# Optimization experiments

Hardware: AMD Instinct MI355X
Metric: run time of the kernel (lower is better)

The kernel has to match this reference:

```python
import jax, jax.numpy as jnp
import numpy as np

# ---- static config (matches init_kwargs) ----
IMG = 56        # num_patches = image_size // patch_size = 112 // 2
WIN = 7         # window_size
SHIFT = 3       # shift_size
C = 256         # projection_dim
H = 8           # num_heads
DH = C // H     # head dim = 32
S = WIN * WIN   # tokens per window = 49
NY = IMG // WIN # windows per side = 8
NW = NY * NY    # windows per image = 64
NMLP = 1024
EPS = 1e-5
SCALE = DH ** (-0.5)


def _relative_position_index():
    ch, cw = np.meshgrid(np.arange(WIN), np.arange(WIN), indexing='ij')
    coords = np.stack([ch, cw]).reshape(2, -1)                 # [2, S]
    rel = coords[:, :, None] - coords[:, None, :]              # [2, S, S]
    rel = rel.transpose(1, 2, 0) + (WIN - 1)                   # [S, S, 2]
    idx = rel[:, :, 0] * (2 * WIN - 1) + rel[:, :, 1]          # [S, S]
    return idx.reshape(-1)                                     # [S*S]

REL_IDX = jnp.asarray(_relative_position_index(), dtype=jnp.int32)


def _attn_mask():
    # Faithful replication of the module's mask construction (incl. the empty
    h_slices = (slice(0, -WIN), slice(-WIN, -SHIFT), slice(-SHIFT, None))
    w_slices = (slice(0, -WIN), slice(-WIN, -WIN), slice(-SHIFT, None))
    m = np.zeros((IMG, IMG), dtype=np.float32)
    count = 0
    for hs in h_slices:
        for ws in w_slices:
            m[hs, ws] = count
            count += 1
    mw = m.reshape(NY, WIN, NY, WIN).transpose(0, 2, 1, 3).reshape(NW, S)
    diff = mw[:, None, :] - mw[:, :, None]
    return np.where(diff != 0, -100.0, 0.0).astype(np.float32)  # [NW, S, S]

ATTN_MASK = jnp.asarray(_attn_mask())


def _layernorm(x, gamma, beta):
    mu = jnp.mean(x, axis=-1, keepdims=True)
    var = jnp.mean(jnp.square(x - mu), axis=-1, keepdims=True)
    return (x - mu) * jax.lax.rsqrt(var + EPS) * gamma + beta


def setup_inputs() -> dict:
    key = jax.random.key(0)
    ks = jax.random.split(key, 12)
    B = 32
    s = lambda fan: 1.0 / np.sqrt(fan)
    return {
        'x': jax.random.normal(ks[0], (B, IMG * IMG, C), dtype=jnp.float32),
        'norm_gamma': jnp.ones((C,), jnp.float32),
        'norm_beta': jnp.zeros((C,), jnp.float32),
        'qkv_w': jax.random.normal(ks[1], (C, 3 * C), jnp.float32) * s(C),
        'qkv_b': jnp.zeros((3 * C,), jnp.float32),
        'proj_w': jax.random.normal(ks[2], (C, C), jnp.float32) * s(C),
        'proj_b': jnp.zeros((C,), jnp.float32),
        'rel_bias_table': jax.random.truncated_normal(ks[3], -2.0, 2.0, ((2 * WIN - 1) ** 2, H), jnp.float32) * 0.02,
        'mlp_w1': jax.random.normal(ks[4], (C, NMLP), jnp.float32) * s(C),
        'mlp_b1': jnp.zeros((NMLP,), jnp.float32),
        'mlp_w2': jax.random.normal(ks[5], (NMLP, C), jnp.float32) * s(NMLP),
        'mlp_b2': jnp.zeros((C,), jnp.float32),
    }


def reference(x, norm_gamma, norm_beta, qkv_w, qkv_b, proj_w, proj_b,
              rel_bias_table, mlp_w1, mlp_b1, mlp_w2, mlp_b2):
    B = x.shape[0]
    # ---- shifted-window attention block ----
    shortcut = x
    xn = _layernorm(x, norm_gamma, norm_beta).reshape(B, IMG, IMG, C)
    shifted = jnp.roll(xn, shift=(-SHIFT, -SHIFT), axis=(1, 2))
    # window partition -> [B*NW, S, C]
    xw = shifted.reshape(B, NY, WIN, NY, WIN, C).transpose(0, 1, 3, 2, 4, 5)
    xw = xw.reshape(B * NW, S, C)
    qkv = xw @ qkv_w + qkv_b                                    # [BnW, S, 3C]
    qkv = qkv.reshape(B * NW, S, 3, H, DH).transpose(2, 0, 3, 1, 4)
    q, k, v = qkv[0] * SCALE, qkv[1], qkv[2]                    # [BnW, H, S, DH]
    attn = jnp.einsum('whsd,whtd->whst', q, k)                  # [BnW, H, S, S]
    bias = rel_bias_table[REL_IDX].reshape(S, S, H).transpose(2, 0, 1)
    attn = attn + bias[None]
    attn = attn.reshape(B, NW, H, S, S) + ATTN_MASK[None, :, None]
    attn = jax.nn.softmax(attn.reshape(B * NW, H, S, S), axis=-1)
    out = jnp.einsum('whst,whtd->wshd', attn, v).reshape(B * NW, S, C)
    out = out @ proj_w + proj_b
    # window reverse + unshift
    out = out.reshape(B, NY, NY, WIN, WIN, C).transpose(0, 1, 3, 2, 4, 5)
    out = out.reshape(B, IMG, IMG, C)
    out = jnp.roll(out, shift=(SHIFT, SHIFT), axis=(1, 2)).reshape(B, IMG * IMG, C)
    x = shortcut + out
    # ---- MLP block (same LayerNorm weights reused, as in original) ----
    shortcut2 = x
    xn2 = _layernorm(x, norm_gamma, norm_beta)
    h = jax.nn.gelu(xn2 @ mlp_w1 + mlp_b1, approximate=False)
    h = h @ mlp_w2 + mlp_b2
    return shortcut2 + h
```

## Files before the change

### kernel.cpp

```cpp
#include <hip/hip_runtime.h>
#include <math.h>

#define IMG   56
#define WINSZ 7
#define SHIFTSZ 3
#define CDIM  256
#define NH    8
#define DH    32
#define SEQ   49
#define NYW   8
#define NWIN  64
#define NMLP  1024
#define BATCH 32
#define NTOK  (BATCH*IMG*IMG)
#define BNW   (BATCH*NWIN)
#define SZT   ((size_t)NTOK*CDIM)
#define QSCALE 0.17677669529663687f
#define EPSLN 1e-5f

typedef __attribute__((ext_vector_type(8))) short short8;
typedef __attribute__((ext_vector_type(4))) float f32x4;

__device__ __forceinline__ float bf2f(unsigned short u) {
    union { unsigned i; float f; } c; c.i = ((unsigned)u) << 16; return c.f;
}
__device__ __forceinline__ unsigned short f2bf(float f) {
    union { float f; unsigned i; } c; c.f = f;
    unsigned r = c.i + 0x7fffu + ((c.i >> 16) & 1u);
    return (unsigned short)(r >> 16);
}

__device__ __forceinline__ float gelu_f(float v) {
    float u = v * 0.70710678118654752f;
    float x = fabsf(u);
    float t = __builtin_amdgcn_rcpf(fmaf(0.3275911f, x, 1.0f));
    float e = __expf(-u * u);
    float p = fmaf(1.061405429f, t, -1.453152027f);
    p = fmaf(p, t, 1.421413741f);
    p = fmaf(p, t, -0.284496736f);
    p = fmaf(p, t, 0.254829592f);
    float er = 1.0f - p * t * e;
    er = copysignf(er, u);
    return 0.5f * v * (1.0f + er);
}

#define GLL16(gp, lp) __builtin_amdgcn_global_load_lds( \
    (__attribute__((address_space(1))) void*)(gp),      \
    (__attribute__((address_space(3))) void*)(lp), 16, 0, 0)

__global__ __launch_bounds__(256) void wtrans(const float* __restrict__ in,
                                              unsigned short* __restrict__ out,
                                              int K, int N) {
    int idx = blockIdx.x * 256 + threadIdx.x;
    if (idx >= K * N) return;
    int n = idx / K, k = idx - n * K;
    out[idx] = f2bf(in[(size_t)k * N + n]);
}

template<int WINDOWED>
__global__ __launch_bounds__(256) void ln_kernel(const float* __restrict__ x,
                                                 const float* __restrict__ gamma,
                                                 const float* __restrict__ beta,
                                                 unsigned short* __restrict__ out) {
    int wave = threadIdx.x >> 6;
    int lane = threadIdx.x & 63;
    int tok  = blockIdx.x * 4 + wave;
    int src  = tok;
    if (WINDOWED) {
        int b  = tok / (NWIN * SEQ);
        int r  = tok - b * (NWIN * SEQ);
        int wl = r / SEQ, s = r - wl * SEQ;
        int wy = wl >> 3, wx = wl & 7;
        int i  = s / WINSZ, j = s - i * WINSZ;
        int hp = wy * WINSZ + i + SHIFTSZ; if (hp >= IMG) hp -= IMG;
        int wp = wx * WINSZ + j + SHIFTSZ; if (wp >= IMG) wp -= IMG;
        src = b * (IMG * IMG) + hp * IMG + wp;
    }
    float4 v = *(const float4*)(x + (size_t)src * CDIM + lane * 4);
    float sum = v.x + v.y + v.z + v.w;
    float ss  = v.x*v.x + v.y*v.y + v.z*v.z + v.w*v.w;
#pragma unroll
    for (int off = 32; off; off >>= 1) {
        sum += __shfl_xor(sum, off);
        ss  += __shfl_xor(ss,  off);
    }
    float mu   = sum * (1.0f / CDIM);
    float var  = ss * (1.0f / CDIM) - mu * mu;
    float rstd = rsqrtf(var + EPSLN);
    float4 g  = *(const float4*)(gamma + lane * 4);
    float4 be = *(const float4*)(beta  + lane * 4);
    ushort4 o;
    o.x = f2bf((v.x - mu) * rstd * g.x + be.x);
    o.y = f2bf((v.y - mu) * rstd * g.y + be.y);
    o.z = f2bf((v.z - mu) * rstd * g.z + be.z);
    o.w = f2bf((v.w - mu) * rstd * g.w + be.w);
    *(ushort4*)(out + (size_t)tok * CDIM + lane * 4) = o;
}

#define EPI_QKV  0
#define EPI_PROJ 1
#define EPI_MLP1 2
#define EPI_MLP2 3

template<int EPI>
__global__ __launch_bounds__(256)
void gemm_bt(const unsigned short* __restrict__ A,
             const unsigned short* __restrict__ Bt,
             int K,
             const float* __restrict__ bias,
             const float* __restrict__ resin,
             float* __restrict__ outF,
             unsigned short* __restrict__ outH) {
    __shared__ __align__(16) unsigned short As[128 * 32];
    __shared__ __align__(16) unsigned short Bs[128 * 32];
    int tid  = threadIdx.x;
    int lane = tid & 63, wave = tid >> 6;
    int q4   = lane >> 4, l16 = lane & 15;
    int wm   = wave >> 1, wn = wave & 1;
    int rowBase = blockIdx.y * 128;
    int colBase = blockIdx.x * 128;

    f32x4 acc[4][4];
#pragma unroll
    for (int i = 0; i < 4; i++)
#pragma unroll
        for (int j = 0; j < 4; j++) acc[i][j] = (f32x4){0.f, 0.f, 0.f, 0.f};

    const unsigned short* Ab = A  + (size_t)rowBase * K;
    const unsigned short* Bb = Bt + (size_t)colBase * K;

    int r0 = wave * 32;
    int ra = r0 + (lane >> 2);
    int rb = ra + 16;
    int ca = (lane & 3) ^ ((ra >> 1) & 3);
    int cb = (lane & 3) ^ ((rb >> 1) & 3);
    const size_t off1 = (size_t)ra * K + ca * 8;
    const size_t off2 = (size_t)rb * K + cb * 8;
    unsigned short* ldsA1 = &As[r0 * 32];
    unsigned short* ldsA2 = &As[(r0 + 16) * 32];
    unsigned short* ldsB1 = &Bs[r0 * 32];
    unsigned short* ldsB2 = &Bs[(r0 + 16) * 32];

    for (int k0 = 0; k0 < K; k0 += 32) {
        __syncthreads();
        GLL16(Ab + off1 + k0, ldsA1);
        GLL16(Ab + off2 + k0, ldsA2);
        GLL16(Bb + off1 + k0, ldsB1);
        GLL16(Bb + off2 + k0, ldsB2);
        __syncthreads();
        short8 af[4], bf[4];
#pragma unroll
        for (int mi = 0; mi < 4; mi++) {
            int r = wm * 64 + mi * 16 + l16;
            af[mi] = *(const short8*)&As[r * 32 + ((q4 ^ ((r >> 1) & 3)) * 8)];
        }
#pragma unroll
        for (int ni = 0; ni < 4; ni++) {
            int r = wn * 64 + ni * 16 + l16;
            bf[ni] = *(const short8*)&Bs[r * 32 + ((q4 ^ ((r >> 1) & 3)) * 8)];
        }
#pragma unroll
        for (int mi = 0; mi < 4; mi++)
#pragma unroll
            for (int ni = 0; ni < 4; ni++)
                acc[mi][ni] = __builtin_amdgcn_mfma_f32_16x16x32_bf16(
                    bf[ni], af[mi], acc[mi][ni], 0, 0, 0);
    }

    int mb = rowBase + wm * 64;
    int nb = colBase + wn * 64;
    float4 bias4[4];
#pragma unroll
    for (int ni = 0; ni < 4; ni++)
        bias4[ni] = *(const float4*)(bias + nb + ni * 16 + q4 * 4);

    if (EPI == EPI_QKV) {
        int three = colBase >> 8;
#pragma unroll
        for (int mi = 0; mi < 4; mi++) {
            int m = mb + mi * 16 + l16;
            int w = m / SEQ, s = m - w * SEQ;
#pragma unroll
            for (int ni = 0; ni < 4; ni++) {
                int n0 = nb + ni * 16 + q4 * 4;
                int hh = (n0 >> 5) & 7, dd0 = n0 & 31;
                const float* bp = (const float*)&bias4[ni];
                if (three == 2) {
#pragma unroll
                    for (int r = 0; r < 4; r++)
                        outH[2 * SZT + (((size_t)(w * NH + hh)) * DH + dd0 + r) * 64 + s] =
                            f2bf(acc[mi][ni][r] + bp[r]);
                } else {
                    float sc = (three == 0) ? QSCALE : 1.0f;
                    ushort4 o;
                    o.x = f2bf((acc[mi][ni][0] + bp[0]) * sc);
                    o.y = f2bf((acc[mi][ni][1] + bp[1]) * sc);
                    o.z = f2bf((acc[mi][ni][2] + bp[2]) * sc);
                    o.w = f2bf((acc[mi][ni][3] + bp[3]) * sc);
                    *(ushort4*)(outH + (size_t)three * SZT +
                                (((size_t)(w * NH + hh)) * SEQ + s) * DH + dd0) = o;
                }
            }
        }
    } else if (EPI == EPI_PROJ) {
#pragma unroll
        for (int mi = 0; mi < 4; mi++) {
            int m = mb + mi * 16 + l16;
            int w = m / SEQ, s = m - w * SEQ;
            int b = w >> 6, wl = w & 63;
            int wy = wl >> 3, wx = wl & 7;
            int ii = s / WINSZ, jj = s - ii * WINSZ;
            int hp = wy * WINSZ + ii + SHIFTSZ; if (hp >= IMG) hp -= IMG;
            int wp = wx * WINSZ + jj + SHIFTSZ; if (wp >= IMG) wp -= IMG;
            size_t tok = (size_t)b * (IMG * IMG) + hp * IMG + wp;
#pragma unroll
            for (int ni = 0; ni < 4; ni++) {
                int n0 = nb + ni * 16 + q4 * 4;
                float4 res = *(const float4*)(resin + tok * CDIM + n0);
                float4 o;
                o.x = acc[mi][ni][0] + bias4[ni].x + res.x;
                o.y = acc[mi][ni][1] + bias4[ni].y + res.y;
                o.z = acc[mi][ni][2] + bias4[ni].z + res.z;
                o.w = acc[mi][ni][3] + bias4[ni].w + res.w;
                *(float4*)(outF + tok * CDIM + n0) = o;
            }
        }
    } else if (EPI == EPI_MLP1) {
#pragma unroll
        for (int mi = 0; mi < 4; mi++) {
            int m = mb + mi * 16 + l16;
#pragma unroll
            for (int ni = 0; ni < 4; ni++) {
                int n0 = nb + ni * 16 + q4 * 4;
                ushort4 o;
                o.x = f2bf(gelu_f(acc[mi][ni][0] + bias4[ni].x));
                o.y = f2bf(gelu_f(acc[mi][ni][1] + bias4[ni].y));
                o.z = f2bf(gelu_f(acc[mi][ni][2] + bias4[ni].z));
                o.w = f2bf(gelu_f(acc[mi][ni][3] + bias4[ni].w));
                *(ushort4*)(outH + (size_t)m * NMLP + n0) = o;
            }
        }
    } else {
#pragma unroll
        for (int mi = 0; mi < 4; mi++) {
            int m = mb + mi * 16 + l16;
#pragma unroll
            for (int ni = 0; ni < 4; ni++) {
                int n0 = nb + ni * 16 + q4 * 4;
                float4 res = *(const float4*)(resin + (size_t)m * CDIM + n0);
                float4 o;
                o.x = acc[mi][ni][0] + bias4[ni].x + res.x;
                o.y = acc[mi][ni][1] + bias4[ni].y + res.y;
                o.z = acc[mi][ni][2] + bias4[ni].z + res.z;
                o.w = acc[mi][ni][3] + bias4[ni].w + res.w;
                *(float4*)(outF + (size_t)m * CDIM + n0) = o;
            }
        }
    }
}

__global__ __launch_bounds__(256) void attn_mfma(const unsigned short* __restrict__ qb,
                                                 const unsigned short* __restrict__ kb,
                                                 const unsigned short* __restrict__ vT,
                                                 const float* __restrict__ rel_tab,
                                                 unsigned short* __restrict__ outp) {
    __shared__ __align__(16) unsigned short Pl[4][64 * 64];
    __shared__ float tab[4][169];
    int tid  = threadIdx.x;
    int wave = tid >> 6, lane = tid & 63;
    int q4   = lane >> 4, l16 = lane & 15;
    int job  = blockIdx.x * 4 + wave;
    int w    = job >> 3, h = job & 7;

    for (int i = lane; i < 169; i += 64) tab[wave][i] = rel_tab[i * NH + h];

    const unsigned short* qg = qb + (size_t)(w * NH + h) * SEQ * DH;
    const unsigned short* kg = kb + (size_t)(w * NH + h) * SEQ * DH;
    short8 aq[4], bk[4];
#pragma unroll
    for (int mi = 0; mi < 4; mi++)
        aq[mi] = *(const short8*)(qg + (mi * 16 + l16) * DH + q4 * 8);
#pragma unroll
    for (int ni = 0; ni < 4; ni++)
        bk[ni] = *(const short8*)(kg + (ni * 16 + l16) * DH + q4 * 8);

    f32x4 acc[4][4];
#pragma unroll
    for (int i = 0; i < 4; i++)
#pragma unroll
        for (int j = 0; j < 4; j++) acc[i][j] = (f32x4){0.f, 0.f, 0.f, 0.f};
#pragma unroll
    for (int mi = 0; mi < 4; mi++)
#pragma unroll
        for (int ni = 0; ni < 4; ni++)
            acc[mi][ni] = __builtin_amdgcn_mfma_f32_16x16x32_bf16(
                aq[mi], bk[ni], acc[mi][ni], 0, 0, 0);

    int wl = w & 63;
    int wy = wl >> 3, wx = wl & 7;
    bool edge = (wy == 7) || (wx == 7);

    int itv[4], jtv[4], ltv[4];
#pragma unroll
    for (int ni = 0; ni < 4; ni++) {
        int t  = ni * 16 + l16;
        int it = (t * 37) >> 8;
        int jt = t - it * 7;
        itv[ni] = it; jtv[ni] = jt;
        int lab;
        if (wx == 7 && jt < 4) lab = 0;
        else {
            int lh = (wy == 7) ? ((it < 4) ? 1 : 2) : 0;
            lab = lh * 3 + ((wx == 7) ? 2 : 0);
        }
        ltv[ni] = lab;
    }

    float rinv[4][4];
#pragma unroll
    for (int mi = 0; mi < 4; mi++) {
#pragma unroll
        for (int r = 0; r < 4; r++) {
            int s  = mi * 16 + q4 * 4 + r;
            int is = (s * 37) >> 8;
            int js = s - is * 7;
            int lab_s;
            if (wx == 7 && js < 4) lab_s = 0;
            else {
                int lh = (wy == 7) ? ((is < 4) ? 1 : 2) : 0;
                lab_s = lh * 3 + ((wx == 7) ? 2 : 0);
            }
            float vv[4];
#pragma unroll
            for (int ni = 0; ni < 4; ni++) {
                int t = ni * 16 + l16;
                float a = acc[mi][ni][r];
                if (t < SEQ) {
                    int idx = (is - itv[ni] + 6) * 13 + (js - jtv[ni] + 6);
                    idx = idx < 0 ? 0 : (idx > 168 ? 168 : idx);
                    a += tab[wave][idx];
                    if (edge && lab_s != ltv[ni]) a -= 100.0f;
                } else {
                    a = -1e30f;
                }
                vv[ni] = a;
            }
            float mx = fmaxf(fmaxf(vv[0], vv[1]), fmaxf(vv[2], vv[3]));
#pragma unroll
            for (int off = 1; off < 16; off <<= 1) mx = fmaxf(mx, __shfl_xor(mx, off));
            float sm = 0.0f;
            unsigned short pb[4];
#pragma unroll
            for (int ni = 0; ni < 4; ni++) {
                float p = __expf(vv[ni] - mx);
                sm += p;
                pb[ni] = f2bf(p);
            }
#pragma unroll
            for (int off = 1; off < 16; off <<= 1) sm += __shfl_xor(sm, off);
            rinv[mi][r] = 1.0f / sm;
#pragma unroll
            for (int ni = 0; ni < 4; ni++) {
                int t  = ni * 16 + l16;
                int kbk = t >> 3, j = t & 7;
                Pl[wave][s * 64 + ((kbk ^ (s & 7)) * 8) + j] = pb[ni];
            }
        }
    }
    __syncthreads();

    short8 pa[4][2];
#pragma unroll
    for (int mi = 0; mi < 4; mi++)
#pragma unroll
        for (int ks = 0; ks < 2; ks++) {
            int m  = mi * 16 + l16;
            int kbk = ks * 4 + q4;
            pa[mi][ks] = *(const short8*)&Pl[wave][m * 64 + ((kbk ^ (m & 7)) * 8)];
        }
    const unsigned short* vg = vT + (size_t)(w * NH + h) * DH * 64;
    short8 bv[2][2];
#pragma unroll
    for (int n2 = 0; n2 < 2; n2++)
#pragma unroll
        for (int ks = 0; ks < 2; ks++)
            bv[n2][ks] = *(const short8*)(vg + (n2 * 16 + l16) * 64 + ks * 32 + q4 * 8);

    f32x4 o[4][2];
#pragma unroll
    for (int mi = 0; mi < 4; mi++)
#pragma unroll
        for (int n2 = 0; n2 < 2; n2++) o[mi][n2] = (f32x4){0.f, 0.f, 0.f, 0.f};
#pragma unroll
    for (int ks = 0; ks < 2; ks++)
#pragma unroll
        for (int mi = 0; mi < 4; mi++)
#pragma unroll
            for (int n2 = 0; n2 < 2; n2++)
                o[mi][n2] = __builtin_amdgcn_mfma_f32_16x16x32_bf16(
                    pa[mi][ks], bv[n2][ks], o[mi][n2], 0, 0, 0);

#pragma unroll
    for (int mi = 0; mi < 4; mi++)
#pragma unroll
        for (int r = 0; r < 4; r++) {
            int s = mi * 16 + q4 * 4 + r;
            if (s < SEQ) {
#pragma unroll
                for (int n2 = 0; n2 < 2; n2++) {
                    int d = n2 * 16 + l16;
                    outp[((size_t)w * SEQ + s) * CDIM + h * DH + d] =
                        f2bf(o[mi][n2][r] * rinv[mi][r]);
                }
            }
        }
}

extern "C" void kernel_launch(void* const* d_in, const int* in_sizes, int n_in,
                              void* d_out, int out_size, void* d_ws, size_t ws_size,
                              hipStream_t stream) {
    const float* x      = (const float*)d_in[0];
    const float* gamma  = (const float*)d_in[1];
    const float* beta   = (const float*)d_in[2];
    const float* qkv_w  = (const float*)d_in[3];
    const float* qkv_b  = (const float*)d_in[4];
    const float* proj_w = (const float*)d_in[5];
    const float* proj_b = (const float*)d_in[6];
    const float* rel_t  = (const float*)d_in[7];
    const float* mlp_w1 = (const float*)d_in[8];
    const float* mlp_b1 = (const float*)d_in[9];
    const float* mlp_w2 = (const float*)d_in[10];
    const float* mlp_b2 = (const float*)d_in[11];
    float* outp = (float*)d_out;

    const size_t VTSZ = (size_t)BNW * NH * DH * 64;
    unsigned short* xw_bf   = (unsigned short*)d_ws;
    unsigned short* qkv_bf  = xw_bf + SZT;
    unsigned short* attn_bf = qkv_bf + 2 * SZT + VTSZ;
    float*          y1      = (float*)(attn_bf + SZT);
    unsigned short* wt_bf   = (unsigned short*)(y1 + SZT);
    unsigned short* h_bf    = qkv_bf;

    unsigned short* qkvW  = wt_bf;
    unsigned short* projW = qkvW  + 768 * 256;
    unsigned short* mlp1W = projW + 256 * 256;
    unsigned short* mlp2W = mlp1W + 1024 * 256;

    wtrans<<<(768 * 256 + 255) / 256, 256, 0, stream>>>(qkv_w, qkvW, CDIM, 3 * CDIM);
    wtrans<<<(256 * 256 + 255) / 256, 256, 0, stream>>>(proj_w, projW, CDIM, CDIM);
    wtrans<<<(1024 * 256 + 255) / 256, 256, 0, stream>>>(mlp_w1, mlp1W, CDIM, NMLP);
    wtrans<<<(256 * 1024 + 255) / 256, 256, 0, stream>>>(mlp_w2, mlp2W, NMLP, CDIM);

    ln_kernel<1><<<NTOK / 4, 256, 0, stream>>>(x, gamma, beta, xw_bf);
    gemm_bt<EPI_QKV><<<dim3(6, NTOK / 128), 256, 0, stream>>>(
        xw_bf, qkvW, CDIM, qkv_b, nullptr, nullptr, qkv_bf);
    attn_mfma<<<BNW * NH / 4, 256, 0, stream>>>(
        qkv_bf, qkv_bf + SZT, qkv_bf + 2 * SZT, rel_t, attn_bf);
    gemm_bt<EPI_PROJ><<<dim3(2, NTOK / 128), 256, 0, stream>>>(
        attn_bf, projW, CDIM, proj_b, x, y1, nullptr);
    ln_kernel<0><<<NTOK / 4, 256, 0, stream>>>(y1, gamma, beta, xw_bf);
    gemm_bt<EPI_MLP1><<<dim3(8, NTOK / 128), 256, 0, stream>>>(
        xw_bf, mlp1W, CDIM, mlp_b1, nullptr, nullptr, h_bf);
    gemm_bt<EPI_MLP2><<<dim3(2, NTOK / 128), 256, 0, stream>>>(
        h_bf, mlp2W, NMLP, mlp_b2, y1, outp, nullptr);
}
```

Baseline: 758.0 us.

## Load GEMM fragments directly from global memory with register double buffering

Drops the LDS staging (global_load_lds into shared tiles plus two barriers per K step) in the bf16 GEMM. Each wave now reads its MFMA operand fragments straight from global memory into registers and prefetches the next 32-wide K slice while the current one computes. This removes the barriers and LDS traffic, but waves that share a tile now load the same A/B rows redundantly from global/L2. Each global read is 16 bytes per lane spread across 16 rows, so coalescing is poorer, and the extra fragment buffers raise register pressure.

Measured after the change: 1.085 ms. 43.2% more time.

```diff
diff --git a/kernel.cpp b/kernel.cpp
--- a/kernel.cpp
+++ b/kernel.cpp
@@ -43,10 +43,6 @@
     er = copysignf(er, u);
     return 0.5f * v * (1.0f + er);
 }
-
-#define GLL16(gp, lp) __builtin_amdgcn_global_load_lds( \
-    (__attribute__((address_space(1))) void*)(gp),      \
-    (__attribute__((address_space(3))) void*)(lp), 16, 0, 0)
 
 __global__ __launch_bounds__(256) void wtrans(const float* __restrict__ in,
                                               unsigned short* __restrict__ out,
@@ -111,8 +107,6 @@
              const float* __restrict__ resin,
              float* __restrict__ outF,
              unsigned short* __restrict__ outH) {
-    __shared__ __align__(16) unsigned short As[128 * 32];
-    __shared__ __align__(16) unsigned short Bs[128 * 32];
     int tid  = threadIdx.x;
     int lane = tid & 63, wave = tid >> 6;
     int q4   = lane >> 4, l16 = lane & 15;
@@ -120,51 +114,45 @@
     int rowBase = blockIdx.y * 128;
     int colBase = blockIdx.x * 128;
 
+    const unsigned short* Ap = A  + (size_t)(rowBase + wm * 64 + l16) * K + q4 * 8;
+    const unsigned short* Bp = Bt + (size_t)(colBase + wn * 64 + l16) * K + q4 * 8;
+    const size_t aStride = (size_t)16 * K;
+
     f32x4 acc[4][4];
 #pragma unroll
     for (int i = 0; i < 4; i++)
 #pragma unroll
         for (int j = 0; j < 4; j++) acc[i][j] = (f32x4){0.f, 0.f, 0.f, 0.f};
 
-    const unsigned short* Ab = A  + (size_t)rowBase * K;
-    const unsigned short* Bb = Bt + (size_t)colBase * K;
-
-    int r0 = wave * 32;
-    int ra = r0 + (lane >> 2);
-    int rb = ra + 16;
-    int ca = (lane & 3) ^ ((ra >> 1) & 3);
-    int cb = (lane & 3) ^ ((rb >> 1) & 3);
-    const size_t off1 = (size_t)ra * K + ca * 8;
-    const size_t off2 = (size_t)rb * K + cb * 8;
-    unsigned short* ldsA1 = &As[r0 * 32];
-    unsigned short* ldsA2 = &As[(r0 + 16) * 32];
-    unsigned short* ldsB1 = &Bs[r0 * 32];
-    unsigned short* ldsB2 = &Bs[(r0 + 16) * 32];
-
-    for (int k0 = 0; k0 < K; k0 += 32) {
-        __syncthreads();
-        GLL16(Ab + off1 + k0, ldsA1);
-        GLL16(Ab + off2 + k0, ldsA2);
-        GLL16(Bb + off1 + k0, ldsB1);
-        GLL16(Bb + off2 + k0, ldsB2);
-        __syncthreads();
-        short8 af[4], bf[4];
-#pragma unroll
-        for (int mi = 0; mi < 4; mi++) {
-            int r = wm * 64 + mi * 16 + l16;
-            af[mi] = *(const short8*)&As[r * 32 + ((q4 ^ ((r >> 1) & 3)) * 8)];
-        }
-#pragma unroll
-        for (int ni = 0; ni < 4; ni++) {
-            int r = wn * 64 + ni * 16 + l16;
-            bf[ni] = *(const short8*)&Bs[r * 32 + ((q4 ^ ((r >> 1) & 3)) * 8)];
-        }
+    short8 a0[4], b0[4], a1[4], b1[4];
+#pragma unroll
+    for (int mi = 0; mi < 4; mi++) a0[mi] = *(const short8*)(Ap + mi * aStride);
+#pragma unroll
+    for (int ni = 0; ni < 4; ni++) b0[ni] = *(const short8*)(Bp + ni * aStride);
+
+    for (int k0 = 0; k0 < K; k0 += 64) {
+        int k1 = k0 + 32;
+        int k2 = (k0 + 64 < K) ? k0 + 64 : 0;
+#pragma unroll
+        for (int mi = 0; mi < 4; mi++) a1[mi] = *(const short8*)(Ap + mi * aStride + k1);
+#pragma unroll
+        for (int ni = 0; ni < 4; ni++) b1[ni] = *(const short8*)(Bp + ni * aStride + k1);
 #pragma unroll
         for (int mi = 0; mi < 4; mi++)
 #pragma unroll
             for (int ni = 0; ni < 4; ni++)
                 acc[mi][ni] = __builtin_amdgcn_mfma_f32_16x16x32_bf16(
-                    bf[ni], af[mi], acc[mi][ni], 0, 0, 0);
+                    b0[ni], a0[mi], acc[mi][ni], 0, 0, 0);
+#pragma unroll
+        for (int mi = 0; mi < 4; mi++) a0[mi] = *(const short8*)(Ap + mi * aStride + k2);
+#pragma unroll
+        for (int ni = 0; ni < 4; ni++) b0[ni] = *(const short8*)(Bp + ni * aStride + k2);
+#pragma unroll
+        for (int mi = 0; mi < 4; mi++)
+#pragma unroll
+            for (int ni = 0; ni < 4; ni++)
+                acc[mi][ni] = __builtin_amdgcn_mfma_f32_16x16x32_bf16(
+                    b1[ni], a1[mi], acc[mi][ni], 0, 0, 0);
     }
 
     int mb = rowBase + wm * 64;
```
